# Optimization experiments

Hardware: AMD Instinct MI355X
Metric: run time of the kernel (lower is better)

## Reference

```python
import jax, jax.numpy as jnp
import numpy as np

USER_SIZE = 100000
ITEM_SIZE = 50000
LATENT = 256
BATCH = 8192
ALPHA = 0.8
TAU = 3.0
SHRINK_NORM = 1.0


def setup_inputs() -> dict:
    key = jax.random.key(0)
    k1, k2, k3, k4 = jax.random.split(key, 4)
    # xavier-uniform style init like the torch code
    bu = np.sqrt(6.0 / (USER_SIZE + LATENT)).astype(np.float32)
    bi = np.sqrt(6.0 / (ITEM_SIZE + LATENT)).astype(np.float32)
    user_embed = jax.random.uniform(k1, (USER_SIZE, LATENT), jnp.float32, -bu, bu)
    item_embed = jax.random.uniform(k2, (ITEM_SIZE, LATENT), jnp.float32, -bi, bi)
    u = jax.random.randint(k3, (BATCH,), 0, USER_SIZE)
    p = jax.random.randint(k4, (BATCH,), 0, ITEM_SIZE)
    return {"user_embed": user_embed, "item_embed": item_embed, "u": u, "p": p}


def _spec_smooth(x):
    # x: [B, d] row-normalized embeddings
    # x - alpha * softmax(x x^T * tau, axis=1) @ x, then shrink-norm rescale
    attn = jax.nn.softmax(jnp.einsum('bd,cd->bc', x, x) * TAU, axis=1)  # [B, B]
    y = x - ALPHA * (attn @ x)
    # shrink_norm != 0 branch (static config)
    norm = jnp.linalg.norm(y, axis=1, keepdims=True)
    return y * (norm * SHRINK_NORM)


def reference(user_embed, item_embed, u, p):
    fu = user_embed[u]
    fp = item_embed[p]
    fu = fu / jnp.linalg.norm(fu, axis=1, keepdims=True)
    fp = fp / jnp.linalg.norm(fp, axis=1, keepdims=True)
    fu = _spec_smooth(fu)
    fp = _spec_smooth(fp)
    out = jax.nn.sigmoid(jnp.sum(fu * fp, axis=1))  # [B]
    return -jnp.sum(jnp.log(out)) / BATCH
```

## Files before the change

### kernel.cpp

```cpp
#include <hip/hip_runtime.h>
#include <hip/hip_bf16.h>

#define B_ROWS 8192
#define D_DIM  256
#define QB     64
#define KB     64
#define NT     (B_ROWS / KB)
#define ALPHA  0.8f
#define TAU_LOG2E 4.328085122666890f

typedef __attribute__((ext_vector_type(8))) short bf16x8;
typedef __attribute__((ext_vector_type(4))) float f32x4;
typedef __attribute__((ext_vector_type(4))) unsigned short ushort4v;

__device__ inline unsigned short f2bf(float f) {
    unsigned int u = __builtin_bit_cast(unsigned int, f);
    u += 0x7FFF + ((u >> 16) & 1);
    return (unsigned short)(u >> 16);
}

__device__ inline void gl_lds16(const void* g, void* l) {
    __builtin_amdgcn_global_load_lds(
        (const __attribute__((address_space(1))) unsigned int*)g,
        (__attribute__((address_space(3))) unsigned int*)l, 16, 0, 0);
}

__device__ inline void barrier_lgkm() {
    asm volatile("s_waitcnt lgkmcnt(0)" ::: "memory");
    __builtin_amdgcn_s_barrier();
    asm volatile("" ::: "memory");
}
__device__ inline void barrier_all() {
    asm volatile("s_waitcnt vmcnt(0) lgkmcnt(0)" ::: "memory");
    __builtin_amdgcn_s_barrier();
    asm volatile("" ::: "memory");
}

__global__ __launch_bounds__(256) void k_gather_norm(
    const float* __restrict__ ue, const float* __restrict__ ie,
    const int* __restrict__ u, const int* __restrict__ p,
    float* __restrict__ Xf, unsigned short* __restrict__ Xh,
    float* __restrict__ out)
{
    const int b = blockIdx.x * 4 + (threadIdx.x >> 6);
    const int lane = threadIdx.x & 63;
    if (b == 0 && lane == 0) out[0] = 0.0f;
    const int m = b >> 13;
    const int r = b & 8191;
    const float* src = (m == 0) ? (ue + (size_t)u[r] * D_DIM)
                                : (ie + (size_t)p[r] * D_DIM);
    float4 v = ((const float4*)src)[lane];
    float ss = v.x*v.x + v.y*v.y + v.z*v.z + v.w*v.w;
    #pragma unroll
    for (int mask = 32; mask; mask >>= 1) ss += __shfl_xor(ss, mask);
    const float inv = 1.0f / sqrtf(ss);
    v.x *= inv; v.y *= inv; v.z *= inv; v.w *= inv;
    const size_t off = (size_t)(m * B_ROWS + r) * D_DIM + lane * 4;
    *(float4*)(Xf + off) = v;
    ushort4v h = { f2bf(v.x), f2bf(v.y), f2bf(v.z), f2bf(v.w) };
    *(ushort4v*)(Xh + off) = h;
}

__global__ __launch_bounds__(256) void k_transpose(
    const unsigned short* __restrict__ Xh, unsigned short* __restrict__ Xht)
{
    __shared__ unsigned short tile[64 * 84];
    const int bid = blockIdx.x;
    const int m = bid >> 9;
    const int t = bid & 511;
    const int rt = t >> 2, ct = t & 3;
    const int r0 = rt * 64, c0 = ct * 64;
    const int tid = threadIdx.x;
    const unsigned short* src = Xh + (size_t)m * B_ROWS * D_DIM;
    unsigned short* dst = Xht + (size_t)m * D_DIM * B_ROWS;
    #pragma unroll
    for (int ph = 0; ph < 2; ++ph) {
        const int row = ph * 32 + (tid >> 3);
        const int ch = tid & 7;
        const unsigned short* s = src + (size_t)(r0 + row) * D_DIM + c0 + ch * 8;
        ushort4v a = *(const ushort4v*)s;
        ushort4v b = *(const ushort4v*)(s + 4);
        *(ushort4v*)(&tile[row * 84 + ch * 8]) = a;
        *(ushort4v*)(&tile[row * 84 + ch * 8 + 4]) = b;
    }
    __syncthreads();
    #pragma unroll
    for (int ph = 0; ph < 2; ++ph) {
        const int d = ph * 32 + (tid >> 3);
        const int kc = tid & 7;
        ushort4v lo = { tile[(kc*8+0)*84 + d], tile[(kc*8+1)*84 + d],
                        tile[(kc*8+2)*84 + d], tile[(kc*8+3)*84 + d] };
        ushort4v hi = { tile[(kc*8+4)*84 + d], tile[(kc*8+5)*84 + d],
                        tile[(kc*8+6)*84 + d], tile[(kc*8+7)*84 + d] };
        unsigned short* o = dst + (size_t)(c0 + d) * B_ROWS + r0 + kc * 8;
        *(ushort4v*)o = lo;
        *(ushort4v*)(o + 4) = hi;
    }
}

__global__ __launch_bounds__(512, 2) void k_flash(
    const unsigned short* __restrict__ Xh,
    const unsigned short* __restrict__ Xht,
    float* __restrict__ Xf)
{
    __shared__ unsigned char Kls[2][64 * 512];
    __shared__ unsigned char Vtls[2][256 * 128];
    __shared__ unsigned char Pls[64 * 128];
    __shared__ float lsum_sh[4][QB];
    __shared__ float nrm_sh[4][QB];

    const int tid = threadIdx.x;
    const int lane = tid & 63;
    const int w = tid >> 6;
    const int wm = w >> 2;
    const int wn = w & 3;
    const int m = blockIdx.x >> 7;
    const int q0 = (blockIdx.x & 127) * QB;

    const unsigned short* Xm  = Xh  + (size_t)m * B_ROWS * D_DIM;
    const unsigned short* Xtm = Xht + (size_t)m * D_DIM * B_ROWS;
    float* Xfm = Xf + (size_t)m * B_ROWS * D_DIM;

    bf16x8 qf[2][8];
    #pragma unroll
    for (int mi = 0; mi < 2; ++mi) {
        const unsigned short* qb = Xm + (size_t)(q0 + wm*32 + mi*16 + (lane & 15)) * D_DIM
                                      + (lane >> 4) * 8;
        #pragma unroll
        for (int kk = 0; kk < 8; ++kk)
            qf[mi][kk] = *(const bf16x8*)(qb + kk * 32);
    }

    const int kchunk0 = w * 4;
    const int krow_l  = (lane >> 5);
    const int kcol16  = lane & 31;
    const int vd_l    = (lane >> 3);
    const int vkc16   = lane & 7;

    #pragma unroll
    for (int it = 0; it < 4; ++it) {
        const int chunk = kchunk0 + it;
        const int krow = chunk * 2 + krow_l;
        const int kdch = kcol16 ^ (krow & 7);
        gl_lds16(Xm + (size_t)krow * D_DIM + kdch * 8, &Kls[0][chunk * 1024]);
        const int vd = chunk * 8 + vd_l;
        const int vkc = vkc16 ^ (vd & 7);
        gl_lds16(Xtm + (size_t)vd * B_ROWS + vkc * 8, &Vtls[0][chunk * 1024]);
    }
    barrier_all();

    f32x4 o[2][4];
    #pragma unroll
    for (int mi = 0; mi < 2; ++mi)
        #pragma unroll
        for (int nf = 0; nf < 4; ++nf) o[mi][nf] = (f32x4){0.f, 0.f, 0.f, 0.f};
    float lsum[2][4] = {{0.f,0.f,0.f,0.f},{0.f,0.f,0.f,0.f}};
    int cur = 0;

    for (int kt = 0; kt < NT; ++kt) {
        const int nxt = cur ^ 1;
        if (kt + 1 < NT) {
            const int kvn = (kt + 1) * KB;
            #pragma unroll
            for (int it = 0; it < 4; ++it) {
                const int chunk = kchunk0 + it;
                const int krow = chunk * 2 + krow_l;
                const int kdch = kcol16 ^ (krow & 7);
                gl_lds16(Xm + (size_t)(kvn + krow) * D_DIM + kdch * 8,
                         &Kls[nxt][chunk * 1024]);
                const int vd = chunk * 8 + vd_l;
                const int vkc = vkc16 ^ (vd & 7);
                gl_lds16(Xtm + (size_t)vd * B_ROWS + kvn + vkc * 8,
                         &Vtls[nxt][chunk * 1024]);
            }
        }

        f32x4 s0 = {0.f,0.f,0.f,0.f}, s1 = {0.f,0.f,0.f,0.f};
        {
            const int brow = wn * 16 + (lane & 15);
            const unsigned char* kbase = &Kls[cur][brow * 512];
            const int bswz = (brow & 7) << 4;
            #pragma unroll
            for (int kk = 0; kk < 8; ++kk) {
                const int kb = kk * 64 + ((lane >> 4) * 16);
                bf16x8 bK = *(const bf16x8*)(kbase + (kb ^ bswz));
                s0 = __builtin_amdgcn_mfma_f32_16x16x32_bf16(qf[0][kk], bK, s0, 0, 0, 0);
                s1 = __builtin_amdgcn_mfma_f32_16x16x32_bf16(qf[1][kk], bK, s1, 0, 0, 0);
            }
        }
        #pragma unroll
        for (int i = 0; i < 4; ++i) {
            const float p0 = exp2f(s0[i] * TAU_LOG2E);
            const float p1 = exp2f(s1[i] * TAU_LOG2E);
            lsum[0][i] += p0;
            lsum[1][i] += p1;
            const int pr0 = wm*32 + (lane >> 4) * 4 + i;
            const int pr1 = pr0 + 16;
            const int pc2 = (wn*16 + (lane & 15)) * 2;
            *(unsigned short*)(Pls + pr0*128 + (pc2 ^ ((pr0 & 7) << 4))) = f2bf(p0);
            *(unsigned short*)(Pls + pr1*128 + (pc2 ^ ((pr1 & 7) << 4))) = f2bf(p1);
        }
        barrier_lgkm();

        bf16x8 aP[2][2];
        #pragma unroll
        for (int mi = 0; mi < 2; ++mi)
            #pragma unroll
            for (int ks = 0; ks < 2; ++ks) {
                const int ar = wm*32 + mi*16 + (lane & 15);
                const int akb = ks*64 + ((lane >> 4) * 16);
                aP[mi][ks] = *(const bf16x8*)(Pls + ar*128 + (akb ^ ((ar & 7) << 4)));
            }
        #pragma unroll
        for (int ks = 0; ks < 2; ++ks) {
            #pragma unroll
            for (int nf = 0; nf < 4; ++nf) {
                const int dr = wn*64 + nf*16 + (lane & 15);
                const int kb2 = ks*64 + ((lane >> 4) * 16);
                bf16x8 bV = *(const bf16x8*)(&Vtls[cur][dr*128 + (kb2 ^ ((dr & 7) << 4))]);
                o[0][nf] = __builtin_amdgcn_mfma_f32_16x16x32_bf16(aP[0][ks], bV, o[0][nf], 0, 0, 0);
                o[1][nf] = __builtin_amdgcn_mfma_f32_16x16x32_bf16(aP[1][ks], bV, o[1][nf], 0, 0, 0);
            }
        }

        barrier_all();
        cur = nxt;
    }

    #pragma unroll
    for (int mi = 0; mi < 2; ++mi)
        #pragma unroll
        for (int i = 0; i < 4; ++i) {
            float v = lsum[mi][i];
            v += __shfl_xor(v, 1); v += __shfl_xor(v, 2);
            v += __shfl_xor(v, 4); v += __shfl_xor(v, 8);
            if ((lane & 15) == 0)
                lsum_sh[wn][wm*32 + mi*16 + (lane >> 4)*4 + i] = v;
        }
    __syncthreads();

    float nrm[2][4] = {{0.f,0.f,0.f,0.f},{0.f,0.f,0.f,0.f}};
    #pragma unroll
    for (int mi = 0; mi < 2; ++mi)
        #pragma unroll
        for (int nf = 0; nf < 4; ++nf)
            #pragma unroll
            for (int i = 0; i < 4; ++i) {
                const int row = wm*32 + mi*16 + (lane >> 4)*4 + i;
                const int col = wn*64 + nf*16 + (lane & 15);
                const float x = Xfm[(size_t)(q0 + row) * D_DIM + col];
                const float lt = lsum_sh[0][row] + lsum_sh[1][row]
                               + lsum_sh[2][row] + lsum_sh[3][row];
                const float y = x - (ALPHA / lt) * o[mi][nf][i];
                o[mi][nf][i] = y;
                nrm[mi][i] += y * y;
            }
    #pragma unroll
    for (int mi = 0; mi < 2; ++mi)
        #pragma unroll
        for (int i = 0; i < 4; ++i) {
            float v = nrm[mi][i];
            v += __shfl_xor(v, 1); v += __shfl_xor(v, 2);
            v += __shfl_xor(v, 4); v += __shfl_xor(v, 8);
            if ((lane & 15) == 0)
                nrm_sh[wn][wm*32 + mi*16 + (lane >> 4)*4 + i] = v;
        }
    __syncthreads();

    #pragma unroll
    for (int mi = 0; mi < 2; ++mi)
        #pragma unroll
        for (int nf = 0; nf < 4; ++nf)
            #pragma unroll
            for (int i = 0; i < 4; ++i) {
                const int row = wm*32 + mi*16 + (lane >> 4)*4 + i;
                const int col = wn*64 + nf*16 + (lane & 15);
                const float scale = sqrtf(nrm_sh[0][row] + nrm_sh[1][row]
                                        + nrm_sh[2][row] + nrm_sh[3][row]);
                Xfm[(size_t)(q0 + row) * D_DIM + col] = o[mi][nf][i] * scale;
            }
}

__global__ __launch_bounds__(256) void k_loss(
    const float* __restrict__ Yu, const float* __restrict__ Yp,
    float* __restrict__ out)
{
    __shared__ float part[4];
    const int w = threadIdx.x >> 6;
    const int lane = threadIdx.x & 63;
    float acc = 0.0f;
    #pragma unroll
    for (int r = 0; r < 8; ++r) {
        const int row = blockIdx.x * 32 + w * 8 + r;
        const float4 a = *(const float4*)(Yu + (size_t)row * D_DIM + lane * 4);
        const float4 b = *(const float4*)(Yp + (size_t)row * D_DIM + lane * 4);
        float dot = a.x*b.x + a.y*b.y + a.z*b.z + a.w*b.w;
        #pragma unroll
        for (int mask = 32; mask; mask >>= 1) dot += __shfl_xor(dot, mask);
        if (lane == 0) acc += log1pf(expf(-dot));
    }
    if (lane == 0) part[w] = acc;
    __syncthreads();
    if (threadIdx.x == 0) {
        const float s = part[0] + part[1] + part[2] + part[3];
        atomicAdd(out, s * (1.0f / 8192.0f));
    }
}

extern "C" void kernel_launch(void* const* d_in, const int* in_sizes, int n_in,
                              void* d_out, int out_size, void* d_ws, size_t ws_size,
                              hipStream_t stream) {
    const float* ue = (const float*)d_in[0];
    const float* ie = (const float*)d_in[1];
    const int*   u  = (const int*)d_in[2];
    const int*   p  = (const int*)d_in[3];
    float* out = (float*)d_out;

    char* ws = (char*)d_ws;
    float* Xf            = (float*)ws;
    unsigned short* Xh   = (unsigned short*)(ws + (16u << 20));
    unsigned short* Xht  = (unsigned short*)(ws + (24u << 20));

    k_gather_norm<<<4096, 256, 0, stream>>>(ue, ie, u, p, Xf, Xh, out);
    k_transpose <<<1024, 256, 0, stream>>>(Xh, Xht);
    k_flash     <<<256, 512, 0, stream>>>(Xh, Xht, Xf);
    k_loss      <<<256, 256, 0, stream>>>(Xf, Xf + (size_t)B_ROWS * D_DIM, out);
}
```

Baseline: 411.0 us.

## Split attention KV range across two blocks and merge in fused combine-loss kernel

The flash kernel now runs as 512 blocks, each covering half of the key/value rows (split-K). Partial outputs and row sums are written to workspace, and a new combine kernel merges them, applies the residual and norm scaling, and computes the loss in one pass. The per-block LDS pipeline drops from double buffering to a single buffer, and MFMA sections get a raised wave priority. This aims to fill more CUs on a 256-CU device, at the cost of extra partial-output traffic and less overlap of loads with compute inside each block. The old path is kept as a fallback when the workspace is too small.

```diff
diff --git a/kernel.cpp b/kernel.cpp
--- a/kernel.cpp
+++ b/kernel.cpp
@@ -6,6 +6,7 @@
 #define QB     64
 #define KB     64
 #define NT     (B_ROWS / KB)
+#define NT2    (NT / 2)
 #define ALPHA  0.8f
 #define TAU_LOG2E 4.328085122666890f
 
@@ -98,37 +99,39 @@
     }
 }
 
-__global__ __launch_bounds__(512, 2) void k_flash(
+__global__ __launch_bounds__(512, 2) void k_flash_part(
     const unsigned short* __restrict__ Xh,
     const unsigned short* __restrict__ Xht,
-    float* __restrict__ Xf)
+    float* __restrict__ Opart,
+    float* __restrict__ lsum_part)
 {
-    __shared__ unsigned char Kls[2][64 * 512];
-    __shared__ unsigned char Vtls[2][256 * 128];
+    __shared__ unsigned char Kls[64 * 512];
+    __shared__ unsigned char Vtls[256 * 128];
     __shared__ unsigned char Pls[64 * 128];
     __shared__ float lsum_sh[4][QB];
-    __shared__ float nrm_sh[4][QB];
 
     const int tid = threadIdx.x;
     const int lane = tid & 63;
     const int w = tid >> 6;
     const int wm = w >> 2;
     const int wn = w & 3;
-    const int m = blockIdx.x >> 7;
-    const int q0 = (blockIdx.x & 127) * QB;
+    const int m  = blockIdx.x >> 8;
+    const int qb = (blockIdx.x >> 1) & 127;
+    const int h  = blockIdx.x & 1;
+    const int q0 = qb * QB;
+    const int kvbase = h * (B_ROWS / 2);
 
     const unsigned short* Xm  = Xh  + (size_t)m * B_ROWS * D_DIM;
     const unsigned short* Xtm = Xht + (size_t)m * D_DIM * B_ROWS;
-    float* Xfm = Xf + (size_t)m * B_ROWS * D_DIM;
 
     bf16x8 qf[2][8];
     #pragma unroll
     for (int mi = 0; mi < 2; ++mi) {
-        const unsigned short* qb = Xm + (size_t)(q0 + wm*32 + mi*16 + (lane & 15)) * D_DIM
-                                      + (lane >> 4) * 8;
+        const unsigned short* qbp = Xm + (size_t)(q0 + wm*32 + mi*16 + (lane & 15)) * D_DIM
+                                       + (lane >> 4) * 8;
         #pragma unroll
         for (int kk = 0; kk < 8; ++kk)
-            qf[mi][kk] = *(const bf16x8*)(qb + kk * 32);
+            qf[mi][kk] = *(const bf16x8*)(qbp + kk * 32);
     }
 
     const int kchunk0 = w * 4;
@@ -142,12 +145,11 @@
         const int chunk = kchunk0 + it;
         const int krow = chunk * 2 + krow_l;
         const int kdch = kcol16 ^ (krow & 7);
-        gl_lds16(Xm + (size_t)krow * D_DIM + kdch * 8, &Kls[0][chunk * 1024]);
+        gl_lds16(Xm + (size_t)(kvbase + krow) * D_DIM + kdch * 8, &Kls[chunk * 1024]);
         const int vd = chunk * 8 + vd_l;
         const int vkc = vkc16 ^ (vd & 7);
-        gl_lds16(Xtm + (size_t)vd * B_ROWS + vkc * 8, &Vtls[0][chunk * 1024]);
-    }
-    barrier_all();
+        gl_lds16(Xtm + (size_t)vd * B_ROWS + kvbase + vkc * 8, &Vtls[chunk * 1024]);
+    }
 
     f32x4 o[2][4];
     #pragma unroll
@@ -155,31 +157,16 @@
         #pragma unroll
         for (int nf = 0; nf < 4; ++nf) o[mi][nf] = (f32x4){0.f, 0.f, 0.f, 0.f};
     float lsum[2][4] = {{0.f,0.f,0.f,0.f},{0.f,0.f,0.f,0.f}};
-    int cur = 0;
-
-    for (int kt = 0; kt < NT; ++kt) {
-        const int nxt = cur ^ 1;
-        if (kt + 1 < NT) {
-            const int kvn = (kt + 1) * KB;
-            #pragma unroll
-            for (int it = 0; it < 4; ++it) {
-                const int chunk = kchunk0 + it;
-                const int krow = chunk * 2 + krow_l;
-                const int kdch = kcol16 ^ (krow & 7);
-                gl_lds16(Xm + (size_t)(kvn + krow) * D_DIM + kdch * 8,
-                         &Kls[nxt][chunk * 1024]);
-                const int vd = chunk * 8 + vd_l;
-                const int vkc = vkc16 ^ (vd & 7);
-                gl_lds16(Xtm + (size_t)vd * B_ROWS + kvn + vkc * 8,
-                         &Vtls[nxt][chunk * 1024]);
-            }
-        }
+
+    for (int kt = 0; kt < NT2; ++kt) {
+        barrier_all();
 
         f32x4 s0 = {0.f,0.f,0.f,0.f}, s1 = {0.f,0.f,0.f,0.f};
         {
             const int brow = wn * 16 + (lane & 15);
-            const unsigned char* kbase = &Kls[cur][brow * 512];
+            const unsigned char* kbase = &Kls[brow * 512];
             const int bswz = (brow & 7) << 4;
+            __builtin_amdgcn_s_setprio(1);
             #pragma unroll
             for (int kk = 0; kk < 8; ++kk) {
                 const int kb = kk * 64 + ((lane >> 4) * 16);
@@ -187,6 +174,7 @@
                 s0 = __builtin_amdgcn_mfma_f32_16x16x32_bf16(qf[0][kk], bK, s0, 0, 0, 0);
                 s1 = __builtin_amdgcn_mfma_f32_16x16x32_bf16(qf[1][kk], bK, s1, 0, 0, 0);
             }
+            __builtin_amdgcn_s_setprio(0);
         }
         #pragma unroll
         for (int i = 0; i < 4; ++i) {
@@ -211,6 +199,214 @@
                 const int akb = ks*64 + ((lane >> 4) * 16);
                 aP[mi][ks] = *(const bf16x8*)(Pls + ar*128 + (akb ^ ((ar & 7) << 4)));
             }
+        __builtin_amdgcn_s_setprio(1);
+        #pragma unroll
+        for (int ks = 0; ks < 2; ++ks) {
+            #pragma unroll
+            for (int nf = 0; nf < 4; ++nf) {
+                const int dr = wn*64 + nf*16 + (lane & 15);
+                const int kb2 = ks*64 + ((lane >> 4) * 16);
+                bf16x8 bV = *(const bf16x8*)(&Vtls[dr*128 + (kb2 ^ ((dr & 7) << 4))]);
+                o[0][nf] = __builtin_amdgcn_mfma_f32_16x16x32_bf16(aP[0][ks], bV, o[0][nf], 0, 0, 0);
+                o[1][nf] = __builtin_amdgcn_mfma_f32_16x16x32_bf16(aP[1][ks], bV, o[1][nf], 0, 0, 0);
+            }
+        }
+        __builtin_amdgcn_s_setprio(0);
+        barrier_lgkm();
+
+        if (kt + 1 < NT2) {
+            const int kvn = kvbase + (kt + 1) * KB;
+            #pragma unroll
+            for (int it = 0; it < 4; ++it) {
+                const int chunk = kchunk0 + it;
+                const int krow = chunk * 2 + krow_l;
+                const int kdch = kcol16 ^ (krow & 7);
+                gl_lds16(Xm + (size_t)(kvn + krow) * D_DIM + kdch * 8, &Kls[chunk * 1024]);
+                const int vd = chunk * 8 + vd_l;
+                const int vkc = vkc16 ^ (vd & 7);
+                gl_lds16(Xtm + (size_t)vd * B_ROWS + kvn + vkc * 8, &Vtls[chunk * 1024]);
+            }
+        }
+    }
+
+    #pragma unroll
+    for (int mi = 0; mi < 2; ++mi)
+        #pragma unroll
+        for (int i = 0; i < 4; ++i) {
+            float v = lsum[mi][i];
+            v += __shfl_xor(v, 1); v += __shfl_xor(v, 2);
+            v += __shfl_xor(v, 4); v += __shfl_xor(v, 8);
+            if ((lane & 15) == 0)
+                lsum_sh[wn][wm*32 + mi*16 + (lane >> 4)*4 + i] = v;
+        }
+    __syncthreads();
+    if (tid < QB)
+        lsum_part[(size_t)blockIdx.x * QB + tid] =
+            lsum_sh[0][tid] + lsum_sh[1][tid] + lsum_sh[2][tid] + lsum_sh[3][tid];
+
+    float* Ob = Opart + (size_t)blockIdx.x * QB * D_DIM;
+    #pragma unroll
+    for (int mi = 0; mi < 2; ++mi)
+        #pragma unroll
+        for (int nf = 0; nf < 4; ++nf)
+            #pragma unroll
+            for (int i = 0; i < 4; ++i) {
+                const int row = wm*32 + mi*16 + (lane >> 4)*4 + i;
+                const int col = wn*64 + nf*16 + (lane & 15);
+                Ob[row * D_DIM + col] = o[mi][nf][i];
+            }
+}
+
+__global__ __launch_bounds__(256) void k_combine_loss(
+    const float* __restrict__ Xf, const float* __restrict__ Opart,
+    const float* __restrict__ lsum_part, float* __restrict__ out)
+{
+    __shared__ float part[4];
+    const int w = threadIdx.x >> 6;
+    const int lane = threadIdx.x & 63;
+    const int r = blockIdx.x * 4 + w;
+    const int qb = r >> 6, ri = r & 63;
+
+    float y[2][4];
+    float nrm[2];
+    #pragma unroll
+    for (int m = 0; m < 2; ++m) {
+        const int blk0 = m * 256 + qb * 2;
+        const float l = lsum_part[(size_t)blk0 * QB + ri]
+                      + lsum_part[(size_t)(blk0 + 1) * QB + ri];
+        const float c = ALPHA / l;
+        const float4 x  = *(const float4*)(Xf + ((size_t)m * B_ROWS + r) * D_DIM + lane * 4);
+        const float4 o0 = *(const float4*)(Opart + ((size_t)blk0 * QB + ri) * D_DIM + lane * 4);
+        const float4 o1 = *(const float4*)(Opart + ((size_t)(blk0 + 1) * QB + ri) * D_DIM + lane * 4);
+        y[m][0] = x.x - c * (o0.x + o1.x);
+        y[m][1] = x.y - c * (o0.y + o1.y);
+        y[m][2] = x.z - c * (o0.z + o1.z);
+        y[m][3] = x.w - c * (o0.w + o1.w);
+        float s = y[m][0]*y[m][0] + y[m][1]*y[m][1] + y[m][2]*y[m][2] + y[m][3]*y[m][3];
+        #pragma unroll
+        for (int mask = 32; mask; mask >>= 1) s += __shfl_xor(s, mask);
+        nrm[m] = s;
+    }
+    float d = y[0][0]*y[1][0] + y[0][1]*y[1][1] + y[0][2]*y[1][2] + y[0][3]*y[1][3];
+    #pragma unroll
+    for (int mask = 32; mask; mask >>= 1) d += __shfl_xor(d, mask);
+    if (lane == 0) {
+        const float z = sqrtf(nrm[0] * nrm[1]) * d;
+        part[w] = log1pf(expf(-z));
+    }
+    __syncthreads();
+    if (threadIdx.x == 0)
+        atomicAdd(out, (part[0] + part[1] + part[2] + part[3]) * (1.0f / 8192.0f));
+}
+
+__global__ __launch_bounds__(512, 2) void k_flash(
+    const unsigned short* __restrict__ Xh, const unsigned short* __restrict__ Xht,
+    float* __restrict__ Xf)
+{
+    __shared__ unsigned char Kls[2][64 * 512];
+    __shared__ unsigned char Vtls[2][256 * 128];
+    __shared__ unsigned char Pls[64 * 128];
+    __shared__ float lsum_sh[4][QB];
+    __shared__ float nrm_sh[4][QB];
+
+    const int tid = threadIdx.x;
+    const int lane = tid & 63;
+    const int w = tid >> 6;
+    const int wm = w >> 2;
+    const int wn = w & 3;
+    const int m = blockIdx.x >> 7;
+    const int q0 = (blockIdx.x & 127) * QB;
+
+    const unsigned short* Xm  = Xh  + (size_t)m * B_ROWS * D_DIM;
+    const unsigned short* Xtm = Xht + (size_t)m * D_DIM * B_ROWS;
+    float* Xfm = Xf + (size_t)m * B_ROWS * D_DIM;
+
+    bf16x8 qf[2][8];
+    #pragma unroll
+    for (int mi = 0; mi < 2; ++mi) {
+        const unsigned short* qbp = Xm + (size_t)(q0 + wm*32 + mi*16 + (lane & 15)) * D_DIM
+                                       + (lane >> 4) * 8;
+        #pragma unroll
+        for (int kk = 0; kk < 8; ++kk)
+            qf[mi][kk] = *(const bf16x8*)(qbp + kk * 32);
+    }
+
+    const int kchunk0 = w * 4;
+    const int krow_l  = (lane >> 5);
+    const int kcol16  = lane & 31;
+    const int vd_l    = (lane >> 3);
+    const int vkc16   = lane & 7;
+
+    #pragma unroll
+    for (int it = 0; it < 4; ++it) {
+        const int chunk = kchunk0 + it;
+        const int krow = chunk * 2 + krow_l;
+        const int kdch = kcol16 ^ (krow & 7);
+        gl_lds16(Xm + (size_t)krow * D_DIM + kdch * 8, &Kls[0][chunk * 1024]);
+        const int vd = chunk * 8 + vd_l;
+        const int vkc = vkc16 ^ (vd & 7);
+        gl_lds16(Xtm + (size_t)vd * B_ROWS + vkc * 8, &Vtls[0][chunk * 1024]);
+    }
+    barrier_all();
+
+    f32x4 o[2][4];
+    #pragma unroll
+    for (int mi = 0; mi < 2; ++mi)
+        #pragma unroll
+        for (int nf = 0; nf < 4; ++nf) o[mi][nf] = (f32x4){0.f, 0.f, 0.f, 0.f};
+    float lsum[2][4] = {{0.f,0.f,0.f,0.f},{0.f,0.f,0.f,0.f}};
+    int cur = 0;
+
+    for (int kt = 0; kt < NT; ++kt) {
+        const int nxt = cur ^ 1;
+        if (kt + 1 < NT) {
+            const int kvn = (kt + 1) * KB;
+            #pragma unroll
+            for (int it = 0; it < 4; ++it) {
+                const int chunk = kchunk0 + it;
+                const int krow = chunk * 2 + krow_l;
+                const int kdch = kcol16 ^ (krow & 7);
+                gl_lds16(Xm + (size_t)(kvn + krow) * D_DIM + kdch * 8, &Kls[nxt][chunk * 1024]);
+                const int vd = chunk * 8 + vd_l;
+                const int vkc = vkc16 ^ (vd & 7);
+                gl_lds16(Xtm + (size_t)vd * B_ROWS + kvn + vkc * 8, &Vtls[nxt][chunk * 1024]);
+            }
+        }
+        f32x4 s0 = {0.f,0.f,0.f,0.f}, s1 = {0.f,0.f,0.f,0.f};
+        {
+            const int brow = wn * 16 + (lane & 15);
+            const unsigned char* kbase = &Kls[cur][brow * 512];
+            const int bswz = (brow & 7) << 4;
+            #pragma unroll
+            for (int kk = 0; kk < 8; ++kk) {
+                const int kb = kk * 64 + ((lane >> 4) * 16);
+                bf16x8 bK = *(const bf16x8*)(kbase + (kb ^ bswz));
+                s0 = __builtin_amdgcn_mfma_f32_16x16x32_bf16(qf[0][kk], bK, s0, 0, 0, 0);
+                s1 = __builtin_amdgcn_mfma_f32_16x16x32_bf16(qf[1][kk], bK, s1, 0, 0, 0);
+            }
+        }
+        #pragma unroll
+        for (int i = 0; i < 4; ++i) {
+            const float p0 = exp2f(s0[i] * TAU_LOG2E);
+            const float p1 = exp2f(s1[i] * TAU_LOG2E);
+            lsum[0][i] += p0;
+            lsum[1][i] += p1;
+            const int pr0 = wm*32 + (lane >> 4) * 4 + i;
+            const int pr1 = pr0 + 16;
+            const int pc2 = (wn*16 + (lane & 15)) * 2;
+            *(unsigned short*)(Pls + pr0*128 + (pc2 ^ ((pr0 & 7) << 4))) = f2bf(p0);
+            *(unsigned short*)(Pls + pr1*128 + (pc2 ^ ((pr1 & 7) << 4))) = f2bf(p1);
+        }
+        barrier_lgkm();
+        bf16x8 aP[2][2];
+        #pragma unroll
+        for (int mi = 0; mi < 2; ++mi)
+            #pragma unroll
+            for (int ks = 0; ks < 2; ++ks) {
+                const int ar = wm*32 + mi*16 + (lane & 15);
+                const int akb = ks*64 + ((lane >> 4) * 16);
+                aP[mi][ks] = *(const bf16x8*)(Pls + ar*128 + (akb ^ ((ar & 7) << 4)));
+            }
         #pragma unroll
         for (int ks = 0; ks < 2; ++ks) {
             #pragma unroll
@@ -222,7 +418,6 @@
                 o[1][nf] = __builtin_amdgcn_mfma_f32_16x16x32_bf16(aP[1][ks], bV, o[1][nf], 0, 0, 0);
             }
         }
-
         barrier_all();
         cur = nxt;
     }
@@ -251,9 +446,9 @@
                 const float x = Xfm[(size_t)(q0 + row) * D_DIM + col];
                 const float lt = lsum_sh[0][row] + lsum_sh[1][row]
                                + lsum_sh[2][row] + lsum_sh[3][row];
-                const float y = x - (ALPHA / lt) * o[mi][nf][i];
-                o[mi][nf][i] = y;
-                nrm[mi][i] += y * y;
+                const float yv = x - (ALPHA / lt) * o[mi][nf][i];
+                o[mi][nf][i] = yv;
+                nrm[mi][i] += yv * yv;
             }
     #pragma unroll
     for (int mi = 0; mi < 2; ++mi)
@@ -266,7 +461,6 @@
                 nrm_sh[wn][wm*32 + mi*16 + (lane >> 4)*4 + i] = v;
         }
     __syncthreads();
-
     #pragma unroll
     for (int mi = 0; mi < 2; ++mi)
         #pragma unroll
@@ -320,9 +514,18 @@
     float* Xf            = (float*)ws;
     unsigned short* Xh   = (unsigned short*)(ws + (16u << 20));
     unsigned short* Xht  = (unsigned short*)(ws + (24u << 20));
+    float* Opart         = (float*)(ws + (32u << 20));
+    float* lsum_part     = (float*)(ws + (64u << 20));
+
+    const size_t need = (64u << 20) + (128u << 10);
 
     k_gather_norm<<<4096, 256, 0, stream>>>(ue, ie, u, p, Xf, Xh, out);
     k_transpose <<<1024, 256, 0, stream>>>(Xh, Xht);
-    k_flash     <<<256, 512, 0, stream>>>(Xh, Xht, Xf);
-    k_loss      <<<256, 256, 0, stream>>>(Xf, Xf + (size_t)B_ROWS * D_DIM, out);
-}
+    if (ws_size >= need) {
+        k_flash_part  <<<512, 512, 0, stream>>>(Xh, Xht, Opart, lsum_part);
+        k_combine_loss<<<2048, 256, 0, stream>>>(Xf, Opart, lsum_part, out);
+    } else {
+        k_flash<<<256, 512, 0, stream>>>(Xh, Xht, Xf);
+        k_loss <<<256, 256, 0, stream>>>(Xf, Xf + (size_t)B_ROWS * D_DIM, out);
+    }
+}
```

Result: slower. 454.2 us (+10.5%).

## Split attention inner loop into barrier-synchronized phases with staggered K/V prefetch

Applied to the files above, without the earlier changes.

Restructures the flash-style inner loop into explicit phases. K and V tile loads are issued at different points, LDS fragment reads are grouped ahead of the MFMA bursts, and s_setprio raises wave priority during matrix work. The aim is to overlap global-to-LDS transfers and LDS reads with MFMA execution in a ping-pong style schedule. The cost is more workgroup barriers per iteration, which can add stalls. The hand-placed waitcnts also risk subtle ordering bugs.

```diff
diff --git a/kernel.cpp b/kernel.cpp
--- a/kernel.cpp
+++ b/kernel.cpp
@@ -25,15 +25,16 @@
         (__attribute__((address_space(3))) unsigned int*)l, 16, 0, 0);
 }
 
-__device__ inline void barrier_lgkm() {
-    asm volatile("s_waitcnt lgkmcnt(0)" ::: "memory");
+__device__ inline void bar() {
+    asm volatile("" ::: "memory");
     __builtin_amdgcn_s_barrier();
     asm volatile("" ::: "memory");
 }
-__device__ inline void barrier_all() {
-    asm volatile("s_waitcnt vmcnt(0) lgkmcnt(0)" ::: "memory");
-    __builtin_amdgcn_s_barrier();
-    asm volatile("" ::: "memory");
+__device__ inline void wait_lgkm() {
+    asm volatile("s_waitcnt lgkmcnt(0)" ::: "memory");
+}
+__device__ inline void wait_vm() {
+    asm volatile("s_waitcnt vmcnt(0)" ::: "memory");
 }
 
 __global__ __launch_bounds__(256) void k_gather_norm(
@@ -124,11 +125,11 @@
     bf16x8 qf[2][8];
     #pragma unroll
     for (int mi = 0; mi < 2; ++mi) {
-        const unsigned short* qb = Xm + (size_t)(q0 + wm*32 + mi*16 + (lane & 15)) * D_DIM
-                                      + (lane >> 4) * 8;
+        const unsigned short* qbp = Xm + (size_t)(q0 + wm*32 + mi*16 + (lane & 15)) * D_DIM
+                                       + (lane >> 4) * 8;
         #pragma unroll
         for (int kk = 0; kk < 8; ++kk)
-            qf[mi][kk] = *(const bf16x8*)(qb + kk * 32);
+            qf[mi][kk] = *(const bf16x8*)(qbp + kk * 32);
     }
 
     const int kchunk0 = w * 4;
@@ -136,6 +137,12 @@
     const int kcol16  = lane & 31;
     const int vd_l    = (lane >> 3);
     const int vkc16   = lane & 7;
+
+    const int brow  = wn * 16 + (lane & 15);
+    const int bswz  = (brow & 7) << 4;
+    const int kqoff = (lane >> 4) * 16;
+    const int ar0   = wm*32 + (lane & 15);
+    const int ar1   = ar0 + 16;
 
     #pragma unroll
     for (int it = 0; it < 4; ++it) {
@@ -147,7 +154,8 @@
         const int vkc = vkc16 ^ (vd & 7);
         gl_lds16(Xtm + (size_t)vd * B_ROWS + vkc * 8, &Vtls[0][chunk * 1024]);
     }
-    barrier_all();
+    wait_vm();
+    bar();
 
     f32x4 o[2][4];
     #pragma unroll
@@ -159,8 +167,12 @@
 
     for (int kt = 0; kt < NT; ++kt) {
         const int nxt = cur ^ 1;
-        if (kt + 1 < NT) {
-            const int kvn = (kt + 1) * KB;
+        const bool pf = (kt + 1 < NT);
+        const int kvn = (kt + 1) * KB;
+        const unsigned char* Kb = &Kls[cur][brow * 512];
+        const unsigned char* Vb = &Vtls[cur][0];
+
+        if (pf) {
             #pragma unroll
             for (int it = 0; it < 4; ++it) {
                 const int chunk = kchunk0 + it;
@@ -168,26 +180,55 @@
                 const int kdch = kcol16 ^ (krow & 7);
                 gl_lds16(Xm + (size_t)(kvn + krow) * D_DIM + kdch * 8,
                          &Kls[nxt][chunk * 1024]);
+            }
+        }
+        bf16x8 bk0 = *(const bf16x8*)(Kb + ((0*64 + kqoff) ^ bswz));
+        bf16x8 bk1 = *(const bf16x8*)(Kb + ((1*64 + kqoff) ^ bswz));
+        bf16x8 bk2 = *(const bf16x8*)(Kb + ((2*64 + kqoff) ^ bswz));
+        bf16x8 bk3 = *(const bf16x8*)(Kb + ((3*64 + kqoff) ^ bswz));
+        bar();
+        wait_lgkm();
+        f32x4 s0 = {0.f,0.f,0.f,0.f}, s1 = {0.f,0.f,0.f,0.f};
+        __builtin_amdgcn_s_setprio(1);
+        s0 = __builtin_amdgcn_mfma_f32_16x16x32_bf16(qf[0][0], bk0, s0, 0, 0, 0);
+        s1 = __builtin_amdgcn_mfma_f32_16x16x32_bf16(qf[1][0], bk0, s1, 0, 0, 0);
+        s0 = __builtin_amdgcn_mfma_f32_16x16x32_bf16(qf[0][1], bk1, s0, 0, 0, 0);
+        s1 = __builtin_amdgcn_mfma_f32_16x16x32_bf16(qf[1][1], bk1, s1, 0, 0, 0);
+        s0 = __builtin_amdgcn_mfma_f32_16x16x32_bf16(qf[0][2], bk2, s0, 0, 0, 0);
+        s1 = __builtin_amdgcn_mfma_f32_16x16x32_bf16(qf[1][2], bk2, s1, 0, 0, 0);
+        s0 = __builtin_amdgcn_mfma_f32_16x16x32_bf16(qf[0][3], bk3, s0, 0, 0, 0);
+        s1 = __builtin_amdgcn_mfma_f32_16x16x32_bf16(qf[1][3], bk3, s1, 0, 0, 0);
+        __builtin_amdgcn_s_setprio(0);
+        bar();
+
+        if (pf) {
+            #pragma unroll
+            for (int it = 0; it < 4; ++it) {
+                const int chunk = kchunk0 + it;
                 const int vd = chunk * 8 + vd_l;
                 const int vkc = vkc16 ^ (vd & 7);
                 gl_lds16(Xtm + (size_t)vd * B_ROWS + kvn + vkc * 8,
                          &Vtls[nxt][chunk * 1024]);
             }
         }
-
-        f32x4 s0 = {0.f,0.f,0.f,0.f}, s1 = {0.f,0.f,0.f,0.f};
-        {
-            const int brow = wn * 16 + (lane & 15);
-            const unsigned char* kbase = &Kls[cur][brow * 512];
-            const int bswz = (brow & 7) << 4;
-            #pragma unroll
-            for (int kk = 0; kk < 8; ++kk) {
-                const int kb = kk * 64 + ((lane >> 4) * 16);
-                bf16x8 bK = *(const bf16x8*)(kbase + (kb ^ bswz));
-                s0 = __builtin_amdgcn_mfma_f32_16x16x32_bf16(qf[0][kk], bK, s0, 0, 0, 0);
-                s1 = __builtin_amdgcn_mfma_f32_16x16x32_bf16(qf[1][kk], bK, s1, 0, 0, 0);
-            }
-        }
+        bf16x8 bk4 = *(const bf16x8*)(Kb + ((4*64 + kqoff) ^ bswz));
+        bf16x8 bk5 = *(const bf16x8*)(Kb + ((5*64 + kqoff) ^ bswz));
+        bf16x8 bk6 = *(const bf16x8*)(Kb + ((6*64 + kqoff) ^ bswz));
+        bf16x8 bk7 = *(const bf16x8*)(Kb + ((7*64 + kqoff) ^ bswz));
+        bar();
+        wait_lgkm();
+        __builtin_amdgcn_s_setprio(1);
+        s0 = __builtin_amdgcn_mfma_f32_16x16x32_bf16(qf[0][4], bk4, s0, 0, 0, 0);
+        s1 = __builtin_amdgcn_mfma_f32_16x16x32_bf16(qf[1][4], bk4, s1, 0, 0, 0);
+        s0 = __builtin_amdgcn_mfma_f32_16x16x32_bf16(qf[0][5], bk5, s0, 0, 0, 0);
+        s1 = __builtin_amdgcn_mfma_f32_16x16x32_bf16(qf[1][5], bk5, s1, 0, 0, 0);
+        s0 = __builtin_amdgcn_mfma_f32_16x16x32_bf16(qf[0][6], bk6, s0, 0, 0, 0);
+        s1 = __builtin_amdgcn_mfma_f32_16x16x32_bf16(qf[1][6], bk6, s1, 0, 0, 0);
+        s0 = __builtin_amdgcn_mfma_f32_16x16x32_bf16(qf[0][7], bk7, s0, 0, 0, 0);
+        s1 = __builtin_amdgcn_mfma_f32_16x16x32_bf16(qf[1][7], bk7, s1, 0, 0, 0);
+        __builtin_amdgcn_s_setprio(0);
+        bar();
+
         #pragma unroll
         for (int i = 0; i < 4; ++i) {
             const float p0 = exp2f(s0[i] * TAU_LOG2E);
@@ -200,30 +241,60 @@
             *(unsigned short*)(Pls + pr0*128 + (pc2 ^ ((pr0 & 7) << 4))) = f2bf(p0);
             *(unsigned short*)(Pls + pr1*128 + (pc2 ^ ((pr1 & 7) << 4))) = f2bf(p1);
         }
-        barrier_lgkm();
-
-        bf16x8 aP[2][2];
-        #pragma unroll
-        for (int mi = 0; mi < 2; ++mi)
-            #pragma unroll
-            for (int ks = 0; ks < 2; ++ks) {
-                const int ar = wm*32 + mi*16 + (lane & 15);
-                const int akb = ks*64 + ((lane >> 4) * 16);
-                aP[mi][ks] = *(const bf16x8*)(Pls + ar*128 + (akb ^ ((ar & 7) << 4)));
-            }
-        #pragma unroll
-        for (int ks = 0; ks < 2; ++ks) {
-            #pragma unroll
-            for (int nf = 0; nf < 4; ++nf) {
-                const int dr = wn*64 + nf*16 + (lane & 15);
-                const int kb2 = ks*64 + ((lane >> 4) * 16);
-                bf16x8 bV = *(const bf16x8*)(&Vtls[cur][dr*128 + (kb2 ^ ((dr & 7) << 4))]);
-                o[0][nf] = __builtin_amdgcn_mfma_f32_16x16x32_bf16(aP[0][ks], bV, o[0][nf], 0, 0, 0);
-                o[1][nf] = __builtin_amdgcn_mfma_f32_16x16x32_bf16(aP[1][ks], bV, o[1][nf], 0, 0, 0);
-            }
-        }
-
-        barrier_all();
+        bf16x8 v0, v1, v2, v3;
+        {
+            const int dr0 = wn*64 + 0*16 + (lane & 15);
+            const int dr1 = wn*64 + 1*16 + (lane & 15);
+            const int dr2 = wn*64 + 2*16 + (lane & 15);
+            const int dr3 = wn*64 + 3*16 + (lane & 15);
+            v0 = *(const bf16x8*)(Vb + dr0*128 + ((0*64 + kqoff) ^ ((dr0 & 7) << 4)));
+            v1 = *(const bf16x8*)(Vb + dr1*128 + ((0*64 + kqoff) ^ ((dr1 & 7) << 4)));
+            v2 = *(const bf16x8*)(Vb + dr2*128 + ((0*64 + kqoff) ^ ((dr2 & 7) << 4)));
+            v3 = *(const bf16x8*)(Vb + dr3*128 + ((0*64 + kqoff) ^ ((dr3 & 7) << 4)));
+        }
+        wait_lgkm();
+        bar();
+        bf16x8 a00 = *(const bf16x8*)(Pls + ar0*128 + ((0*64 + kqoff) ^ ((ar0 & 7) << 4)));
+        bf16x8 a10 = *(const bf16x8*)(Pls + ar1*128 + ((0*64 + kqoff) ^ ((ar1 & 7) << 4)));
+        wait_lgkm();
+        __builtin_amdgcn_s_setprio(1);
+        o[0][0] = __builtin_amdgcn_mfma_f32_16x16x32_bf16(a00, v0, o[0][0], 0, 0, 0);
+        o[1][0] = __builtin_amdgcn_mfma_f32_16x16x32_bf16(a10, v0, o[1][0], 0, 0, 0);
+        o[0][1] = __builtin_amdgcn_mfma_f32_16x16x32_bf16(a00, v1, o[0][1], 0, 0, 0);
+        o[1][1] = __builtin_amdgcn_mfma_f32_16x16x32_bf16(a10, v1, o[1][1], 0, 0, 0);
+        o[0][2] = __builtin_amdgcn_mfma_f32_16x16x32_bf16(a00, v2, o[0][2], 0, 0, 0);
+        o[1][2] = __builtin_amdgcn_mfma_f32_16x16x32_bf16(a10, v2, o[1][2], 0, 0, 0);
+        o[0][3] = __builtin_amdgcn_mfma_f32_16x16x32_bf16(a00, v3, o[0][3], 0, 0, 0);
+        o[1][3] = __builtin_amdgcn_mfma_f32_16x16x32_bf16(a10, v3, o[1][3], 0, 0, 0);
+        __builtin_amdgcn_s_setprio(0);
+        bar();
+
+        bf16x8 a01 = *(const bf16x8*)(Pls + ar0*128 + ((1*64 + kqoff) ^ ((ar0 & 7) << 4)));
+        bf16x8 a11 = *(const bf16x8*)(Pls + ar1*128 + ((1*64 + kqoff) ^ ((ar1 & 7) << 4)));
+        bf16x8 v4, v5, v6, v7;
+        {
+            const int dr0 = wn*64 + 0*16 + (lane & 15);
+            const int dr1 = wn*64 + 1*16 + (lane & 15);
+            const int dr2 = wn*64 + 2*16 + (lane & 15);
+            const int dr3 = wn*64 + 3*16 + (lane & 15);
+            v4 = *(const bf16x8*)(Vb + dr0*128 + ((1*64 + kqoff) ^ ((dr0 & 7) << 4)));
+            v5 = *(const bf16x8*)(Vb + dr1*128 + ((1*64 + kqoff) ^ ((dr1 & 7) << 4)));
+            v6 = *(const bf16x8*)(Vb + dr2*128 + ((1*64 + kqoff) ^ ((dr2 & 7) << 4)));
+            v7 = *(const bf16x8*)(Vb + dr3*128 + ((1*64 + kqoff) ^ ((dr3 & 7) << 4)));
+        }
+        wait_lgkm();
+        __builtin_amdgcn_s_setprio(1);
+        o[0][0] = __builtin_amdgcn_mfma_f32_16x16x32_bf16(a01, v4, o[0][0], 0, 0, 0);
+        o[1][0] = __builtin_amdgcn_mfma_f32_16x16x32_bf16(a11, v4, o[1][0], 0, 0, 0);
+        o[0][1] = __builtin_amdgcn_mfma_f32_16x16x32_bf16(a01, v5, o[0][1], 0, 0, 0);
+        o[1][1] = __builtin_amdgcn_mfma_f32_16x16x32_bf16(a11, v5, o[1][1], 0, 0, 0);
+        o[0][2] = __builtin_amdgcn_mfma_f32_16x16x32_bf16(a01, v6, o[0][2], 0, 0, 0);
+        o[1][2] = __builtin_amdgcn_mfma_f32_16x16x32_bf16(a11, v6, o[1][2], 0, 0, 0);
+        o[0][3] = __builtin_amdgcn_mfma_f32_16x16x32_bf16(a01, v7, o[0][3], 0, 0, 0);
+        o[1][3] = __builtin_amdgcn_mfma_f32_16x16x32_bf16(a11, v7, o[1][3], 0, 0, 0);
+        __builtin_amdgcn_s_setprio(0);
+        wait_vm();
+        bar();
         cur = nxt;
     }
 
@@ -251,9 +322,9 @@
                 const float x = Xfm[(size_t)(q0 + row) * D_DIM + col];
                 const float lt = lsum_sh[0][row] + lsum_sh[1][row]
                                + lsum_sh[2][row] + lsum_sh[3][row];
-                const float y = x - (ALPHA / lt) * o[mi][nf][i];
-                o[mi][nf][i] = y;
-                nrm[mi][i] += y * y;
+                const float yv = x - (ALPHA / lt) * o[mi][nf][i];
+                o[mi][nf][i] = yv;
+                nrm[mi][i] += yv * yv;
             }
     #pragma unroll
     for (int mi = 0; mi < 2; ++mi)
@@ -266,7 +337,6 @@
                 nrm_sh[wn][wm*32 + mi*16 + (lane >> 4)*4 + i] = v;
         }
     __syncthreads();
-
     #pragma unroll
     for (int mi = 0; mi < 2; ++mi)
         #pragma unroll
```

Result: slower. 419.8 us (+2.1%).
